# Kernel optimization log

Measured on AMD Instinct MI355X. Metric: run time of the kernel, lower is better.

## Reference

```python
import jax, jax.numpy as jnp
import numpy as np

D_MODEL, D_K, D_V, H = 1024, 64, 64, 16
B, NQ, NK = 4, 1024, 1024
HID = D_MODEL // 2


def _dwg(x, W1, b1, W2, b2):
    # DynamicWeightGenerator: sigmoid(fc2(relu(fc1(x))))
    h = jax.nn.relu(jnp.einsum('bnd,hd->bnh', x, W1) + b1)
    return jax.nn.sigmoid(jnp.einsum('bnh,dh->bnd', h, W2) + b2)


def setup_inputs() -> dict:
    key = jax.random.key(0)
    ks = jax.random.split(key, 32)
    s = 0.02
    inp = {
        'queries': jax.random.normal(ks[0], (B, NQ, D_MODEL), jnp.float32),
        'keys': jax.random.normal(ks[1], (B, NK, D_MODEL), jnp.float32),
        'values': jax.random.normal(ks[2], (B, NK, D_MODEL), jnp.float32),
        'attention_mask': jax.random.randint(ks[3], (B, 1, NQ, NK), 0, 2) > 0,
        'attention_weights': jax.random.uniform(ks[4], (B, H, NQ, NK), jnp.float32),
        'memory': jax.random.normal(ks[5], (B, NK), jnp.float32),
        # projections (torch Linear convention: y = x @ W.T + b)
        'Wq': jax.random.normal(ks[6], (H * D_K, D_MODEL), jnp.float32) * s,
        'bq': jnp.zeros((H * D_K,), jnp.float32),
        'Wk': jax.random.normal(ks[7], (H * D_K, D_MODEL), jnp.float32) * s,
        'bk': jnp.zeros((H * D_K,), jnp.float32),
        'Wv': jax.random.normal(ks[8], (H * D_V, D_MODEL), jnp.float32) * s,
        'bv': jnp.zeros((H * D_V,), jnp.float32),
        'Wo': jax.random.normal(ks[9], (D_MODEL, H * D_V), jnp.float32) * s,
        'bo': jnp.zeros((D_MODEL,), jnp.float32),
        'Wmm': jax.random.normal(ks[10], (H * D_V, 1), jnp.float32) * s,
        'bmm': jnp.zeros((H * D_V,), jnp.float32),
    }
    for i, tag in enumerate(['q', 'k', 'v']):
        k0, k1 = ks[11 + 2 * i], ks[12 + 2 * i]
        inp[f'W1{tag}'] = jax.random.normal(k0, (HID, D_MODEL), jnp.float32) * s
        inp[f'b1{tag}'] = jnp.zeros((HID,), jnp.float32)
        inp[f'W2{tag}'] = jax.random.normal(k1, (D_MODEL, HID), jnp.float32) * s
        inp[f'b2{tag}'] = jnp.zeros((D_MODEL,), jnp.float32)
    return inp


def reference(queries, keys, values, attention_mask, attention_weights, memory,
              Wq, bq, Wk, bk, Wv, bv, Wo, bo, Wmm, bmm,
              W1q, b1q, W2q, b2q, W1k, b1k, W2k, b2k, W1v, b1v, W2v, b2v):
    b_s, nq = queries.shape[:2]
    nk = keys.shape[1]
    # dynamic elementwise gating of inputs
    q_in = queries * _dwg(queries, W1q, b1q, W2q, b2q)
    k_in = keys * _dwg(keys, W1k, b1k, W2k, b2k)
    v_in = values * _dwg(values, W1v, b1v, W2v, b2v)
    # projections -> (b, h, n, d)
    q = (jnp.einsum('bnd,ed->bne', q_in, Wq) + bq).reshape(b_s, nq, H, D_K).transpose(0, 2, 1, 3)
    k = (jnp.einsum('bnd,ed->bne', k_in, Wk) + bk).reshape(b_s, nk, H, D_K).transpose(0, 2, 1, 3)
    v = (jnp.einsum('bnd,ed->bne', v_in, Wv) + bv).reshape(b_s, nk, H, D_V).transpose(0, 2, 1, 3)
    # per-token memory factor: fc_mm(memory[..., None]) -> (b, h, nk, d_k)
    mm = (memory[..., None] * Wmm[:, 0] + bmm).reshape(b_s, nk, H, D_K).transpose(0, 2, 1, 3)
    att = jnp.einsum('bhqd,bhkd->bhqk', q, k * mm) / np.sqrt(D_K).astype(np.float32)
    att = att * attention_weights                         # custom scaling (slice [:nk] == full)
    att = jnp.where(attention_mask, -jnp.inf, att)        # masked_fill
    att = jax.nn.softmax(att, axis=-1)
    out = jnp.einsum('bhqk,bhkd->bhqd', att, v * mm)      # (b, h, nq, d_v)
    out = out.transpose(0, 2, 1, 3).reshape(b_s, nq, H * D_V)
    return jnp.einsum('bne,de->bnd', out, Wo) + bo
```

## Files before the change

### kernel.cpp

```cpp
#include <hip/hip_runtime.h>
#include <hip/hip_bf16.h>

#define BB    4
#define NN    1024
#define DM    1024
#define HH    16
#define HID   512
#define TT    (BB * NN)

typedef __attribute__((ext_vector_type(8))) short bf16x8;
typedef __attribute__((ext_vector_type(4))) float f32x4;

__device__ __forceinline__ ushort f2bfu(float f) {
    __hip_bfloat16 h = __float2bfloat16(f);
    return __builtin_bit_cast(ushort, h);
}

__device__ __forceinline__ float bfu2f(ushort u) {
    __hip_bfloat16 h = __builtin_bit_cast(__hip_bfloat16, u);
    return __bfloat162float(h);
}

__device__ __forceinline__ f32x4 mfma16(bf16x8 a, bf16x8 b, f32x4 c) {
    return __builtin_amdgcn_mfma_f32_16x16x32_bf16(a, b, c, 0, 0, 0);
}

__device__ __forceinline__ void gll16(const void* g, void* l) {
    __builtin_amdgcn_global_load_lds(
        (const __attribute__((address_space(1))) unsigned int*)g,
        (__attribute__((address_space(3))) unsigned int*)l, 16, 0, 0);
}

__global__ void detect_mask_kernel(const uint4* __restrict__ m,
                                   int n16, int* __restrict__ flags) {
    int stride = blockDim.x * gridDim.x;
    unsigned hi = 0, lo = 0;
    for (int i = blockIdx.x * blockDim.x + threadIdx.x; i < n16; i += stride) {
        uint4 v = m[i];
        unsigned o = v.x | v.y | v.z | v.w;
        lo |= o & 0xFFu;
        hi |= o & 0xFFFFFF00u;
    }
    if (hi) atomicOr(&flags[0], 1);
    if (lo) atomicOr(&flags[1], 1);
}

#define NSEG 13
struct CvtAll { const float* s[NSEG]; ushort* d[NSEG]; int bound[NSEG]; };

__global__ __launch_bounds__(256) void cvt_all(CvtAll a, int total) {
    int stride = blockDim.x * gridDim.x;
    for (int i = blockIdx.x * blockDim.x + threadIdx.x; i < total; i += stride) {
        const float* sp = a.s[0];
        ushort* dp = a.d[0];
        int base = 0;
        #pragma unroll
        for (int k = 1; k < NSEG; ++k) {
            bool ge = i >= a.bound[k - 1];
            sp = ge ? a.s[k] : sp;
            dp = ge ? a.d[k] : dp;
            base = ge ? a.bound[k - 1] : base;
        }
        int j = i - base;
        float4 v = ((const float4*)sp)[j];
        uint2 o;
        o.x = (unsigned)f2bfu(v.x) | ((unsigned)f2bfu(v.y) << 16);
        o.y = (unsigned)f2bfu(v.z) | ((unsigned)f2bfu(v.w) << 16);
        ((uint2*)dp)[j] = o;
    }
}

struct GB {
    const ushort* A[3]; const ushort* W[3];
    const float* bias[3]; void* C[3]; const ushort* X[3];
};

template <int EP, int NF>
__global__ __launch_bounds__(256) void gemm_bf16(
    GB gb, int M, int N, int K,
    const float* __restrict__ mem, const float* __restrict__ Wmm,
    const float* __restrict__ bmm)
{
    __shared__ __align__(16) ushort As[2][128 * 64];
    __shared__ __align__(16) ushort Bs[2][NF * 32 * 64];
    const int z = blockIdx.z;
    const ushort* A = gb.A[z];
    const ushort* W = gb.W[z];
    const float* bias = gb.bias[z];
    void* Cout = gb.C[z];
    const ushort* X = gb.X[z];

    const int tid = threadIdx.x;
    const int lane = tid & 63, w = tid >> 6;
    const int lc = lane & 15, lg = lane >> 4;
    const int m0 = blockIdx.x * 128, n0 = blockIdx.y * (NF * 32);
    const int wm = (w >> 1) * 64, wn = (w & 1) * (NF * 16);
    const int srow = lane >> 3, scol = 8 * ((lane & 7) ^ srow);
    const int swl = (lc & 7) << 3;

    f32x4 acc[4][NF];
    #pragma unroll
    for (int i = 0; i < 4; ++i)
        #pragma unroll
        for (int j = 0; j < NF; ++j)
            acc[i][j] = (f32x4){0.f, 0.f, 0.f, 0.f};

    auto stage = [&](int buf, int k0) {
        #pragma unroll
        for (int ci = 0; ci < 4; ++ci) {
            int c = w + ci * 4;
            gll16(&A[(size_t)(m0 + c * 8 + srow) * K + k0 + scol], &As[buf][c * 512]);
            if (c < NF * 4)
                gll16(&W[(size_t)(n0 + c * 8 + srow) * K + k0 + scol], &Bs[buf][c * 512]);
        }
    };

    stage(0, 0);
    stage(1, 64);
    const int nt = K / 64;

    for (int t = 0; t < nt; ++t) {
        const int cur = t & 1;
        if (t < nt - 1) {
            if constexpr (NF == 4) asm volatile("s_waitcnt vmcnt(8)" ::: "memory");
            else                   asm volatile("s_waitcnt vmcnt(6)" ::: "memory");
        } else {
            asm volatile("s_waitcnt vmcnt(0)" ::: "memory");
        }
        __builtin_amdgcn_sched_barrier(0);
        __builtin_amdgcn_s_barrier();

        bf16x8 af[4][2], bfr[NF][2];
        #pragma unroll
        for (int mi = 0; mi < 4; ++mi) {
            int row = wm + mi * 16 + lc;
            af[mi][0] = *(const bf16x8*)&As[cur][row * 64 + ((lg * 8) ^ swl)];
            af[mi][1] = *(const bf16x8*)&As[cur][row * 64 + ((32 + lg * 8) ^ swl)];
        }
        #pragma unroll
        for (int nj = 0; nj < NF; ++nj) {
            int row = wn + nj * 16 + lc;
            bfr[nj][0] = *(const bf16x8*)&Bs[cur][row * 64 + ((lg * 8) ^ swl)];
            bfr[nj][1] = *(const bf16x8*)&Bs[cur][row * 64 + ((32 + lg * 8) ^ swl)];
        }
        asm volatile("s_waitcnt lgkmcnt(0)" ::: "memory");
        __builtin_amdgcn_sched_barrier(0);
        __builtin_amdgcn_s_barrier();

        if (t + 2 < nt) stage(cur, (t + 2) * 64);

        #pragma unroll
        for (int mi = 0; mi < 4; ++mi)
            #pragma unroll
            for (int nj = 0; nj < NF; ++nj) {
                acc[mi][nj] = mfma16(af[mi][0], bfr[nj][0], acc[mi][nj]);
                acc[mi][nj] = mfma16(af[mi][1], bfr[nj][1], acc[mi][nj]);
            }
    }

    #pragma unroll
    for (int nj = 0; nj < NF; ++nj) {
        int e = n0 + wn + nj * 16 + lc;
        float bv = bias[e];
        float wmv = 0.f, bmv = 0.f;
        if (EP == 7) { wmv = Wmm[e]; bmv = bmm[e]; }
        #pragma unroll
        for (int mi = 0; mi < 4; ++mi) {
            int mbase = m0 + wm + mi * 16 + lg * 4;
            if (EP == 7 && z == 2) {
                ushort u[4];
                #pragma unroll
                for (int r = 0; r < 4; ++r) {
                    float v = (acc[mi][nj][r] + bv) * (mem[mbase + r] * wmv + bmv);
                    u[r] = f2bfu(v);
                }
                int bb = mbase >> 10, n = mbase & 1023;
                size_t off = ((size_t)(bb * HH + (e >> 6)) * 64 + (e & 63)) * NN + n;
                uint2 pk;
                pk.x = (unsigned)u[0] | ((unsigned)u[1] << 16);
                pk.y = (unsigned)u[2] | ((unsigned)u[3] << 16);
                *(uint2*)&((ushort*)Cout)[off] = pk;
            } else {
                #pragma unroll
                for (int r = 0; r < 4; ++r) {
                    int m = mbase + r;
                    float v = acc[mi][nj][r] + bv;
                    if (EP == 1) v = fmaxf(v, 0.f);
                    if (EP == 2) v = bfu2f(X[(size_t)m * N + e]) * (1.f / (1.f + __expf(-v)));
                    if (EP == 7) {
                        if (z == 0) v = v * 0.125f;
                        else        v = v * (mem[m] * wmv + bmv);
                    }
                    size_t off = (size_t)m * N + e;
                    if (EP == 4) ((float*)Cout)[off] = v;
                    else         ((ushort*)Cout)[off] = f2bfu(v);
                }
            }
        }
    }
}

__global__ __launch_bounds__(256) void attn_fast(
    const ushort* __restrict__ qp, const ushort* __restrict__ kp,
    const ushort* __restrict__ vt, const float* __restrict__ aw,
    const unsigned char* __restrict__ maskp, const int* __restrict__ mflags,
    ushort* __restrict__ ob)
{
    const int mode = mflags[0] ? (mflags[1] ? 1 : 2) : 0;
    if (mode != 1) return;

    __shared__ __align__(16) ushort Ks[2][64 * 64];
    __shared__ __align__(16) ushort Vs[2][64 * 64];
    __shared__ __align__(16) float  AWs[2][64 * 64];
    __shared__ __align__(16) unsigned char Ms[2][64 * 64];
    __shared__ __align__(16) ushort Ps[64 * 64];

    const int tid = threadIdx.x, lane = tid & 63, w = tid >> 6;
    const int lc = lane & 15, lg = lane >> 4;
    const int bid = blockIdx.x;
    const int swz = (bid & 7) * 128 + (bid >> 3);
    const int qt = swz & 15, bh = swz >> 4;
    const int b = bh >> 4, h = bh & 15;
    const int q0 = qt * 64, wq = w * 16;
    const int srow = lane >> 3, scol = 8 * ((lane & 7) ^ srow);
    const int swl = (lc & 7) << 3;
    const int qloc = wq + lc;

    const ushort* qrow = &qp[(size_t)(b * NN + q0 + qloc) * DM + h * 64];
    bf16x8 bq0 = *(const bf16x8*)&qrow[lg * 8];
    bf16x8 bq1 = *(const bf16x8*)&qrow[32 + lg * 8];

    auto stage = [&](int buf, int t) {
        const int k0 = t * 64;
        #pragma unroll
        for (int ci = 0; ci < 2; ++ci) {
            int c = w + ci * 4;
            gll16(&kp[(size_t)(b * NN + k0 + c * 8 + srow) * DM + h * 64 + scol],
                  &Ks[buf][c * 512]);
            gll16(&vt[((size_t)bh * 64 + c * 8 + srow) * NN + k0 + scol],
                  &Vs[buf][c * 512]);
        }
        #pragma unroll
        for (int ci = 0; ci < 4; ++ci) {
            int c = w + ci * 4;
            int row = c * 4 + (lane >> 4);
            int un = (lane & 15) ^ (row & 7);
            gll16(&aw[((size_t)bh * NN + q0 + row) * NN + k0 + un * 4],
                  &AWs[buf][c * 256]);
        }
        {
            int row = w * 16 + (lane >> 2);
            int un = (lane & 3) ^ (row & 3);
            gll16(&maskp[((size_t)b * NN + q0 + row) * NN + k0 + un * 16],
                  &Ms[buf][w * 1024]);
        }
    };

    f32x4 oacc[4];
    #pragma unroll
    for (int i = 0; i < 4; ++i) oacc[i] = (f32x4){0.f, 0.f, 0.f, 0.f};
    float psum = 0.f;

    stage(0, 0);
    stage(1, 1);
    asm volatile("s_waitcnt vmcnt(0)" ::: "memory");
    __builtin_amdgcn_sched_barrier(0);
    __builtin_amdgcn_s_barrier();

    const int awk = qloc & 7;
    const int mkk = qloc & 3;

    for (int t = 0; t < 16; ++t) {
        const int cur = t & 1;
        if (t < 15) asm volatile("s_waitcnt vmcnt(9)" ::: "memory");
        else        asm volatile("s_waitcnt vmcnt(0)" ::: "memory");
        __builtin_amdgcn_sched_barrier(0);
        __builtin_amdgcn_s_barrier();

        bf16x8 af0[4], af1[4], vf0[4], vf1[4];
        float4 awf[4];
        unsigned mkf[4];
        #pragma unroll
        for (int mi = 0; mi < 4; ++mi) {
            int krow = mi * 16 + lc;
            af0[mi] = *(const bf16x8*)&Ks[cur][krow * 64 + ((lg * 8) ^ swl)];
            af1[mi] = *(const bf16x8*)&Ks[cur][krow * 64 + ((32 + lg * 8) ^ swl)];
        }
        #pragma unroll
        for (int nj = 0; nj < 4; ++nj) {
            int vrow = nj * 16 + lc;
            vf0[nj] = *(const bf16x8*)&Vs[cur][vrow * 64 + ((lg * 8) ^ swl)];
            vf1[nj] = *(const bf16x8*)&Vs[cur][vrow * 64 + ((32 + lg * 8) ^ swl)];
        }
        #pragma unroll
        for (int mi = 0; mi < 4; ++mi) {
            awf[mi] = *(const float4*)&AWs[cur][qloc * 64 + (((mi * 4 + lg) ^ awk) * 4)];
            mkf[mi] = *(const unsigned*)&Ms[cur][qloc * 64 + ((mi ^ mkk) * 16) + lg * 4];
        }
        asm volatile("s_waitcnt lgkmcnt(0)" ::: "memory");
        __builtin_amdgcn_sched_barrier(0);
        __builtin_amdgcn_s_barrier();

        if (t + 2 < 16) stage(cur, t + 2);

        f32x4 sacc[4];
        __builtin_amdgcn_s_setprio(1);
        #pragma unroll
        for (int mi = 0; mi < 4; ++mi) {
            f32x4 s = (f32x4){0.f, 0.f, 0.f, 0.f};
            s = mfma16(af0[mi], bq0, s);
            s = mfma16(af1[mi], bq1, s);
            sacc[mi] = s;
        }
        __builtin_amdgcn_s_setprio(0);

        #pragma unroll
        for (int mi = 0; mi < 4; ++mi) {
            unsigned mu = mkf[mi];
            const float aww[4] = {awf[mi].x, awf[mi].y, awf[mi].z, awf[mi].w};
            float pv[4];
            pv[0] = (mu & 0xffu)         ? 0.f : __expf(sacc[mi][0] * aww[0]);
            pv[1] = ((mu >> 8) & 0xffu)  ? 0.f : __expf(sacc[mi][1] * aww[1]);
            pv[2] = ((mu >> 16) & 0xffu) ? 0.f : __expf(sacc[mi][2] * aww[2]);
            pv[3] = ((mu >> 24) & 0xffu) ? 0.f : __expf(sacc[mi][3] * aww[3]);
            psum += pv[0] + pv[1] + pv[2] + pv[3];
            uint2 pk;
            pk.x = (unsigned)f2bfu(pv[0]) | ((unsigned)f2bfu(pv[1]) << 16);
            pk.y = (unsigned)f2bfu(pv[2]) | ((unsigned)f2bfu(pv[3]) << 16);
            *(uint2*)&Ps[qloc * 64 + ((mi * 16 + lg * 4) ^ swl)] = pk;
        }

        __builtin_amdgcn_s_setprio(1);
        {
            bf16x8 pa0 = *(const bf16x8*)&Ps[qloc * 64 + ((lg * 8) ^ swl)];
            #pragma unroll
            for (int nj = 0; nj < 4; ++nj)
                oacc[nj] = mfma16(pa0, vf0[nj], oacc[nj]);
            bf16x8 pa1 = *(const bf16x8*)&Ps[qloc * 64 + ((32 + lg * 8) ^ swl)];
            #pragma unroll
            for (int nj = 0; nj < 4; ++nj)
                oacc[nj] = mfma16(pa1, vf1[nj], oacc[nj]);
        }
        __builtin_amdgcn_s_setprio(0);
    }

    psum += __shfl_xor(psum, 16);
    psum += __shfl_xor(psum, 32);
    float inv = 1.0f / psum;
    float invr[4];
    #pragma unroll
    for (int r = 0; r < 4; ++r)
        invr[r] = __shfl(inv, (lane & 48) | (lg * 4 + r));

    #pragma unroll
    for (int nj = 0; nj < 4; ++nj)
        #pragma unroll
        for (int r = 0; r < 4; ++r) {
            int qq = q0 + wq + lg * 4 + r;
            float v = oacc[nj][r] * invr[r];
            ob[(size_t)(b * NN + qq) * DM + h * 64 + nj * 16 + lc] = f2bfu(v);
        }
}

__global__ __launch_bounds__(256) void attn_mfma_fb(
    const ushort* __restrict__ qp, const ushort* __restrict__ kp,
    const ushort* __restrict__ vt, const float* __restrict__ aw,
    const void* __restrict__ maskp, const int* __restrict__ mflags,
    ushort* __restrict__ ob)
{
    const int mode = mflags[0] ? (mflags[1] ? 1 : 2) : 0;
    if (mode == 1) return;
    __shared__ __align__(16) ushort Ks[2][64 * 64];
    __shared__ __align__(16) ushort Vs[2][64 * 64];
    __shared__ __align__(16) ushort Ps[64 * 64];
    const int tid = threadIdx.x, lane = tid & 63, w = tid >> 6;
    const int lc = lane & 15, lg = lane >> 4;
    const int bid = blockIdx.x;
    const int swz = (bid & 7) * 128 + (bid >> 3);
    const int qt = swz & 15, bh = swz >> 4;
    const int b = bh >> 4, h = bh & 15;
    const int q0 = qt * 64, wq = w * 16;
    const int srow = lane >> 3, scol = 8 * ((lane & 7) ^ srow);
    const int swl = (lc & 7) << 3;

    const ushort* qrow = &qp[(size_t)(b * NN + q0 + wq + lc) * DM + h * 64];
    bf16x8 bq0 = *(const bf16x8*)&qrow[lg * 8];
    bf16x8 bq1 = *(const bf16x8*)&qrow[32 + lg * 8];

    f32x4 oacc[4];
    #pragma unroll
    for (int i = 0; i < 4; ++i) oacc[i] = (f32x4){0.f, 0.f, 0.f, 0.f};
    float psum = 0.f;
    const int q = q0 + wq + lc;
    const float* awrow = aw + ((size_t)bh * NN + q) * NN;
    const size_t mrowo = ((size_t)b * NN + q) * NN;

    float4 awA[4], awB[4];
    uint4 mk4A[4], mk4B[4];

    #pragma unroll
    for (int ci = 0; ci < 2; ++ci) {
        int c = w + ci * 4;
        gll16(&kp[(size_t)(b * NN + c * 8 + srow) * DM + h * 64 + scol], &Ks[0][c * 512]);
        gll16(&vt[((size_t)bh * 64 + c * 8 + srow) * NN + 0 + scol], &Vs[0][c * 512]);
    }
    #pragma unroll
    for (int mi = 0; mi < 4; ++mi) {
        awA[mi] = *(const float4*)&awrow[mi * 16 + lg * 4];
        mk4A[mi] = *(const uint4*)((const char*)maskp + 4 * (mrowo + mi * 16 + lg * 4));
    }
    asm volatile("s_waitcnt vmcnt(0)" ::: "memory");
    __builtin_amdgcn_sched_barrier(0);
    __builtin_amdgcn_s_barrier();

#define ATTN_BODY(T, AWC, MK4C, AWN, MK4N)                                      \
    {                                                                           \
        const int cur = (T) & 1;                                                \
        if ((T) < 15) {                                                         \
            const int kn = ((T) + 1) * 64;                                      \
            _Pragma("unroll")                                                   \
            for (int ci = 0; ci < 2; ++ci) {                                    \
                int c = w + ci * 4;                                             \
                gll16(&kp[(size_t)(b * NN + kn + c * 8 + srow) * DM + h * 64 + scol], \
                      &Ks[cur ^ 1][c * 512]);                                   \
                gll16(&vt[((size_t)bh * 64 + c * 8 + srow) * NN + kn + scol],   \
                      &Vs[cur ^ 1][c * 512]);                                   \
            }                                                                   \
            __builtin_amdgcn_sched_barrier(0);                                  \
            _Pragma("unroll")                                                   \
            for (int mi = 0; mi < 4; ++mi) {                                    \
                AWN[mi] = *(const float4*)&awrow[kn + mi * 16 + lg * 4];        \
                MK4N[mi] = *(const uint4*)((const char*)maskp +                 \
                               4 * (mrowo + kn + mi * 16 + lg * 4));            \
            }                                                                   \
            __builtin_amdgcn_sched_barrier(0);                                  \
        }                                                                       \
        f32x4 sacc[4];                                                          \
        __builtin_amdgcn_s_setprio(1);                                          \
        _Pragma("unroll")                                                       \
        for (int mi = 0; mi < 4; ++mi) {                                        \
            int krow = mi * 16 + lc;                                            \
            bf16x8 a0 = *(const bf16x8*)&Ks[cur][krow * 64 + ((lg * 8) ^ swl)]; \
            bf16x8 a1 = *(const bf16x8*)&Ks[cur][krow * 64 + ((32 + lg * 8) ^ swl)]; \
            f32x4 s = (f32x4){0.f, 0.f, 0.f, 0.f};                              \
            s = mfma16(a0, bq0, s);                                             \
            s = mfma16(a1, bq1, s);                                             \
            sacc[mi] = s;                                                       \
        }                                                                       \
        __builtin_amdgcn_s_setprio(0);                                          \
        _Pragma("unroll")                                                       \
        for (int mi = 0; mi < 4; ++mi) {                                        \
            unsigned mk[4];                                                     \
            if (mode == 0) {                                                    \
                mk[0] = MK4C[mi].x; mk[1] = MK4C[mi].y;                         \
                mk[2] = MK4C[mi].z; mk[3] = MK4C[mi].w;                         \
            } else {                                                            \
                mk[0] = MK4C[mi].x != 0; mk[1] = MK4C[mi].y != 0;               \
                mk[2] = MK4C[mi].z != 0; mk[3] = MK4C[mi].w != 0;               \
            }                                                                   \
            const float aww[4] = {AWC[mi].x, AWC[mi].y, AWC[mi].z, AWC[mi].w};  \
            float pv[4];                                                        \
            _Pragma("unroll")                                                   \
            for (int r = 0; r < 4; ++r) {                                       \
                float sv = sacc[mi][r] * aww[r];                                \
                pv[r] = mk[r] ? 0.f : __expf(sv);                               \
                psum += pv[r];                                                  \
            }                                                                   \
            uint2 pk;                                                           \
            pk.x = (unsigned)f2bfu(pv[0]) | ((unsigned)f2bfu(pv[1]) << 16);     \
            pk.y = (unsigned)f2bfu(pv[2]) | ((unsigned)f2bfu(pv[3]) << 16);     \
            *(uint2*)&Ps[(wq + lc) * 64 + ((mi * 16 + lg * 4) ^ swl)] = pk;     \
        }                                                                       \
        __builtin_amdgcn_s_setprio(1);                                          \
        _Pragma("unroll")                                                       \
        for (int kk = 0; kk < 2; ++kk) {                                        \
            bf16x8 pa = *(const bf16x8*)&Ps[(wq + lc) * 64 + ((kk * 32 + lg * 8) ^ swl)]; \
            _Pragma("unroll")                                                   \
            for (int nj = 0; nj < 4; ++nj) {                                    \
                bf16x8 vb = *(const bf16x8*)&Vs[cur][(nj * 16 + lc) * 64 + ((kk * 32 + lg * 8) ^ swl)]; \
                oacc[nj] = mfma16(pa, vb, oacc[nj]);                            \
            }                                                                   \
        }                                                                       \
        __builtin_amdgcn_s_setprio(0);                                          \
        if ((T) < 15) {                                                         \
            asm volatile("s_waitcnt vmcnt(0)" ::: "memory");                    \
            __builtin_amdgcn_sched_barrier(0);                                  \
            __builtin_amdgcn_s_barrier();                                       \
        }                                                                       \
    }

    for (int tt = 0; tt < 8; ++tt) {
        const int t0 = tt * 2, t1 = tt * 2 + 1;
        ATTN_BODY(t0, awA, mk4A, awB, mk4B);
        ATTN_BODY(t1, awB, mk4B, awA, mk4A);
    }
#undef ATTN_BODY

    psum += __shfl_xor(psum, 16);
    psum += __shfl_xor(psum, 32);
    float inv = 1.0f / psum;
    float invr[4];
    #pragma unroll
    for (int r = 0; r < 4; ++r)
        invr[r] = __shfl(inv, (lane & 48) | (lg * 4 + r));

    #pragma unroll
    for (int nj = 0; nj < 4; ++nj)
        #pragma unroll
        for (int r = 0; r < 4; ++r) {
            int qq = q0 + wq + lg * 4 + r;
            float v = oacc[nj][r] * invr[r];
            ob[(size_t)(b * NN + qq) * DM + h * 64 + nj * 16 + lc] = f2bfu(v);
        }
}

extern "C" void kernel_launch(void* const* d_in, const int* in_sizes, int n_in,
                              void* d_out, int out_size, void* d_ws, size_t ws_size,
                              hipStream_t stream) {
    const float* xin_f[3] = {(const float*)d_in[0], (const float*)d_in[1], (const float*)d_in[2]};
    const void*  maskp   = d_in[3];
    const float* aw      = (const float*)d_in[4];
    const float* memv    = (const float*)d_in[5];
    const float* Wp_f[3] = {(const float*)d_in[6], (const float*)d_in[8], (const float*)d_in[10]};
    const float* bp[3]   = {(const float*)d_in[7], (const float*)d_in[9], (const float*)d_in[11]};
    const float* Wo_f  = (const float*)d_in[12];  const float* bo  = (const float*)d_in[13];
    const float* Wmm = (const float*)d_in[14];    const float* bmm = (const float*)d_in[15];
    const float* W1f[3] = {(const float*)d_in[16], (const float*)d_in[20], (const float*)d_in[24]};
    const float* b1a[3] = {(const float*)d_in[17], (const float*)d_in[21], (const float*)d_in[25]};
    const float* W2f[3] = {(const float*)d_in[18], (const float*)d_in[22], (const float*)d_in[26]};
    const float* b2a[3] = {(const float*)d_in[19], (const float*)d_in[23], (const float*)d_in[27]};

    char* p = (char*)d_ws;
    auto alloc = [&](size_t bytes) { char* r = p; p += (bytes + 255) & ~(size_t)255; return r; };
    int*    mflags = (int*)alloc(256);
    ushort* xbf[3]; for (int t = 0; t < 3; ++t) xbf[t] = (ushort*)alloc((size_t)TT * DM * 2);
    ushort* Wpb[3]; for (int t = 0; t < 3; ++t) Wpb[t] = (ushort*)alloc((size_t)DM * DM * 2);
    ushort* Wob  = (ushort*)alloc((size_t)DM * DM * 2);
    ushort* W1b[3]; for (int t = 0; t < 3; ++t) W1b[t] = (ushort*)alloc((size_t)HID * DM * 2);
    ushort* W2b[3]; for (int t = 0; t < 3; ++t) W2b[t] = (ushort*)alloc((size_t)DM * HID * 2);
    ushort* hbuf[3]; for (int t = 0; t < 3; ++t) hbuf[t] = (ushort*)alloc((size_t)TT * HID * 2);
    ushort* xg[3];  for (int t = 0; t < 3; ++t) xg[t] = (ushort*)alloc((size_t)TT * DM * 2);
    ushort* qpb  = (ushort*)alloc((size_t)TT * DM * 2);
    ushort* ksb  = (ushort*)alloc((size_t)TT * DM * 2);
    ushort* vtb  = (ushort*)alloc((size_t)TT * DM * 2);
    ushort* obuf = (ushort*)alloc((size_t)TT * DM * 2);

    hipMemsetAsync(mflags, 0, 8, stream);
    detect_mask_kernel<<<256, 256, 0, stream>>>((const uint4*)maskp,
                                                BB * NN * NN / 16, mflags);

    {
        CvtAll a;
        const int S_IN = TT * DM / 4, S_W = DM * DM / 4, S_H = HID * DM / 4;
        int idx = 0, cum = 0;
        auto seg = [&](const float* s, ushort* d, int n) {
            a.s[idx] = s; a.d[idx] = d; cum += n; a.bound[idx] = cum; ++idx;
        };
        for (int t = 0; t < 3; ++t) seg(xin_f[t], xbf[t], S_IN);
        for (int t = 0; t < 3; ++t) seg(Wp_f[t], Wpb[t], S_W);
        seg(Wo_f, Wob, S_W);
        for (int t = 0; t < 3; ++t) seg(W1f[t], W1b[t], S_H);
        for (int t = 0; t < 3; ++t) seg(W2f[t], W2b[t], S_H);
        cvt_all<<<2048, 256, 0, stream>>>(a, cum);
    }

    const dim3 blk(256);
    GB g1 = {}, g2 = {}, g3 = {}, g4 = {};
    for (int t = 0; t < 3; ++t) {
        g1.A[t] = xbf[t];  g1.W[t] = W1b[t]; g1.bias[t] = b1a[t]; g1.C[t] = hbuf[t];
        g2.A[t] = hbuf[t]; g2.W[t] = W2b[t]; g2.bias[t] = b2a[t]; g2.C[t] = xg[t]; g2.X[t] = xbf[t];
        g3.A[t] = xg[t];   g3.W[t] = Wpb[t]; g3.bias[t] = bp[t];
    }
    g3.C[0] = qpb; g3.C[1] = ksb; g3.C[2] = vtb;
    g4.A[0] = obuf; g4.W[0] = Wob; g4.bias[0] = bo; g4.C[0] = d_out;

    gemm_bf16<1, 2><<<dim3(TT / 128, HID / 64, 3), blk, 0, stream>>>(g1, TT, HID, DM, nullptr, nullptr, nullptr);
    gemm_bf16<2, 2><<<dim3(TT / 128, DM / 64, 3), blk, 0, stream>>>(g2, TT, DM, HID, nullptr, nullptr, nullptr);
    gemm_bf16<7, 2><<<dim3(TT / 128, DM / 64, 3), blk, 0, stream>>>(g3, TT, DM, DM, memv, Wmm, bmm);

    attn_fast<<<dim3(1024), blk, 0, stream>>>(qpb, ksb, vtb, aw,
                                              (const unsigned char*)maskp, mflags, obuf);
    attn_mfma_fb<<<dim3(1024), blk, 0, stream>>>(qpb, ksb, vtb, aw,
                                                 maskp, mflags, obuf);

    gemm_bf16<4, 2><<<dim3(TT / 128, DM / 64, 1), blk, 0, stream>>>(g4, TT, DM, DM, nullptr, nullptr, nullptr);
}
```

Before: 269.0 us.

## Single-buffer attention LDS tiles and fuse mask detection into convert kernel

Merges the mask-detection pass into the bf16 conversion kernel as extra blocks, removing a separate launch. Converts the attention kernels from double-buffered to single-buffered LDS staging for K, V, attention weights and mask, roughly halving shared memory per block to allow more resident blocks. The next tile's loads are still issued before compute but now need a full wait and barrier each iteration, reducing load/compute overlap within a block.

New measurement: 264.2 us. About the same (-1.8%).

```diff
diff --git a/kernel.cpp b/kernel.cpp
--- a/kernel.cpp
+++ b/kernel.cpp
@@ -31,42 +31,45 @@
         (__attribute__((address_space(3))) unsigned int*)l, 16, 0, 0);
 }
 
-__global__ void detect_mask_kernel(const uint4* __restrict__ m,
-                                   int n16, int* __restrict__ flags) {
-    int stride = blockDim.x * gridDim.x;
-    unsigned hi = 0, lo = 0;
-    for (int i = blockIdx.x * blockDim.x + threadIdx.x; i < n16; i += stride) {
-        uint4 v = m[i];
-        unsigned o = v.x | v.y | v.z | v.w;
-        lo |= o & 0xFFu;
-        hi |= o & 0xFFFFFF00u;
-    }
-    if (hi) atomicOr(&flags[0], 1);
-    if (lo) atomicOr(&flags[1], 1);
-}
-
 #define NSEG 13
 struct CvtAll { const float* s[NSEG]; ushort* d[NSEG]; int bound[NSEG]; };
 
-__global__ __launch_bounds__(256) void cvt_all(CvtAll a, int total) {
-    int stride = blockDim.x * gridDim.x;
-    for (int i = blockIdx.x * blockDim.x + threadIdx.x; i < total; i += stride) {
-        const float* sp = a.s[0];
-        ushort* dp = a.d[0];
-        int base = 0;
-        #pragma unroll
-        for (int k = 1; k < NSEG; ++k) {
-            bool ge = i >= a.bound[k - 1];
-            sp = ge ? a.s[k] : sp;
-            dp = ge ? a.d[k] : dp;
-            base = ge ? a.bound[k - 1] : base;
-        }
-        int j = i - base;
-        float4 v = ((const float4*)sp)[j];
-        uint2 o;
-        o.x = (unsigned)f2bfu(v.x) | ((unsigned)f2bfu(v.y) << 16);
-        o.y = (unsigned)f2bfu(v.z) | ((unsigned)f2bfu(v.w) << 16);
-        ((uint2*)dp)[j] = o;
+__global__ __launch_bounds__(256) void cvt_detect(
+    CvtAll a, int total, const uint4* __restrict__ m, int n16,
+    int* __restrict__ flags)
+{
+    if (blockIdx.x < 2048) {
+        int stride = 256 * 2048;
+        for (int i = blockIdx.x * 256 + threadIdx.x; i < total; i += stride) {
+            const float* sp = a.s[0];
+            ushort* dp = a.d[0];
+            int base = 0;
+            #pragma unroll
+            for (int k = 1; k < NSEG; ++k) {
+                bool ge = i >= a.bound[k - 1];
+                sp = ge ? a.s[k] : sp;
+                dp = ge ? a.d[k] : dp;
+                base = ge ? a.bound[k - 1] : base;
+            }
+            int j = i - base;
+            float4 v = ((const float4*)sp)[j];
+            uint2 o;
+            o.x = (unsigned)f2bfu(v.x) | ((unsigned)f2bfu(v.y) << 16);
+            o.y = (unsigned)f2bfu(v.z) | ((unsigned)f2bfu(v.w) << 16);
+            ((uint2*)dp)[j] = o;
+        }
+    } else {
+        int bid = blockIdx.x - 2048;
+        int stride = 256 * 256;
+        unsigned hi = 0, lo = 0;
+        for (int i = bid * 256 + threadIdx.x; i < n16; i += stride) {
+            uint4 v = m[i];
+            unsigned o = v.x | v.y | v.z | v.w;
+            lo |= o & 0xFFu;
+            hi |= o & 0xFFFFFF00u;
+        }
+        if (hi) atomicOr(&flags[0], 1);
+        if (lo) atomicOr(&flags[1], 1);
     }
 }
 
@@ -209,10 +212,10 @@
     const int mode = mflags[0] ? (mflags[1] ? 1 : 2) : 0;
     if (mode != 1) return;
 
-    __shared__ __align__(16) ushort Ks[2][64 * 64];
-    __shared__ __align__(16) ushort Vs[2][64 * 64];
-    __shared__ __align__(16) float  AWs[2][64 * 64];
-    __shared__ __align__(16) unsigned char Ms[2][64 * 64];
+    __shared__ __align__(16) ushort Ks[64 * 64];
+    __shared__ __align__(16) ushort Vs[64 * 64];
+    __shared__ __align__(16) float  AWs[64 * 64];
+    __shared__ __align__(16) unsigned char Ms[64 * 64];
     __shared__ __align__(16) ushort Ps[64 * 64];
 
     const int tid = threadIdx.x, lane = tid & 63, w = tid >> 6;
@@ -225,20 +228,23 @@
     const int srow = lane >> 3, scol = 8 * ((lane & 7) ^ srow);
     const int swl = (lc & 7) << 3;
     const int qloc = wq + lc;
+    const int awk = qloc & 7, mkk = qloc & 3;
 
     const ushort* qrow = &qp[(size_t)(b * NN + q0 + qloc) * DM + h * 64];
     bf16x8 bq0 = *(const bf16x8*)&qrow[lg * 8];
     bf16x8 bq1 = *(const bf16x8*)&qrow[32 + lg * 8];
 
-    auto stage = [&](int buf, int t) {
+    const unsigned char* mbase = maskp + ((size_t)b * NN + q0) * NN;
+
+    auto stage = [&](int t) {
         const int k0 = t * 64;
         #pragma unroll
         for (int ci = 0; ci < 2; ++ci) {
             int c = w + ci * 4;
             gll16(&kp[(size_t)(b * NN + k0 + c * 8 + srow) * DM + h * 64 + scol],
-                  &Ks[buf][c * 512]);
+                  &Ks[c * 512]);
             gll16(&vt[((size_t)bh * 64 + c * 8 + srow) * NN + k0 + scol],
-                  &Vs[buf][c * 512]);
+                  &Vs[c * 512]);
         }
         #pragma unroll
         for (int ci = 0; ci < 4; ++ci) {
@@ -246,13 +252,12 @@
             int row = c * 4 + (lane >> 4);
             int un = (lane & 15) ^ (row & 7);
             gll16(&aw[((size_t)bh * NN + q0 + row) * NN + k0 + un * 4],
-                  &AWs[buf][c * 256]);
+                  &AWs[c * 256]);
         }
         {
             int row = w * 16 + (lane >> 2);
             int un = (lane & 3) ^ (row & 3);
-            gll16(&maskp[((size_t)b * NN + q0 + row) * NN + k0 + un * 16],
-                  &Ms[buf][w * 1024]);
+            gll16(&mbase[(size_t)row * NN + k0 + un * 16], &Ms[w * 1024]);
         }
     };
 
@@ -261,47 +266,37 @@
     for (int i = 0; i < 4; ++i) oacc[i] = (f32x4){0.f, 0.f, 0.f, 0.f};
     float psum = 0.f;
 
-    stage(0, 0);
-    stage(1, 1);
+    stage(0);
     asm volatile("s_waitcnt vmcnt(0)" ::: "memory");
     __builtin_amdgcn_sched_barrier(0);
     __builtin_amdgcn_s_barrier();
 
-    const int awk = qloc & 7;
-    const int mkk = qloc & 3;
-
     for (int t = 0; t < 16; ++t) {
-        const int cur = t & 1;
-        if (t < 15) asm volatile("s_waitcnt vmcnt(9)" ::: "memory");
-        else        asm volatile("s_waitcnt vmcnt(0)" ::: "memory");
-        __builtin_amdgcn_sched_barrier(0);
-        __builtin_amdgcn_s_barrier();
-
         bf16x8 af0[4], af1[4], vf0[4], vf1[4];
         float4 awf[4];
         unsigned mkf[4];
         #pragma unroll
         for (int mi = 0; mi < 4; ++mi) {
             int krow = mi * 16 + lc;
-            af0[mi] = *(const bf16x8*)&Ks[cur][krow * 64 + ((lg * 8) ^ swl)];
-            af1[mi] = *(const bf16x8*)&Ks[cur][krow * 64 + ((32 + lg * 8) ^ swl)];
+            af0[mi] = *(const bf16x8*)&Ks[krow * 64 + ((lg * 8) ^ swl)];
+            af1[mi] = *(const bf16x8*)&Ks[krow * 64 + ((32 + lg * 8) ^ swl)];
         }
         #pragma unroll
         for (int nj = 0; nj < 4; ++nj) {
             int vrow = nj * 16 + lc;
-            vf0[nj] = *(const bf16x8*)&Vs[cur][vrow * 64 + ((lg * 8) ^ swl)];
-            vf1[nj] = *(const bf16x8*)&Vs[cur][vrow * 64 + ((32 + lg * 8) ^ swl)];
+            vf0[nj] = *(const bf16x8*)&Vs[vrow * 64 + ((lg * 8) ^ swl)];
+            vf1[nj] = *(const bf16x8*)&Vs[vrow * 64 + ((32 + lg * 8) ^ swl)];
         }
         #pragma unroll
         for (int mi = 0; mi < 4; ++mi) {
-            awf[mi] = *(const float4*)&AWs[cur][qloc * 64 + (((mi * 4 + lg) ^ awk) * 4)];
-            mkf[mi] = *(const unsigned*)&Ms[cur][qloc * 64 + ((mi ^ mkk) * 16) + lg * 4];
+            awf[mi] = *(const float4*)&AWs[qloc * 64 + (((mi * 4 + lg) ^ awk) * 4)];
+            mkf[mi] = *(const unsigned*)&Ms[qloc * 64 + ((mi ^ mkk) * 16) + lg * 4];
         }
         asm volatile("s_waitcnt lgkmcnt(0)" ::: "memory");
         __builtin_amdgcn_sched_barrier(0);
         __builtin_amdgcn_s_barrier();
 
-        if (t + 2 < 16) stage(cur, t + 2);
+        if (t < 15) stage(t + 1);
 
         f32x4 sacc[4];
         __builtin_amdgcn_s_setprio(1);
@@ -342,6 +337,12 @@
                 oacc[nj] = mfma16(pa1, vf1[nj], oacc[nj]);
         }
         __builtin_amdgcn_s_setprio(0);
+
+        if (t < 15) {
+            asm volatile("s_waitcnt vmcnt(0)" ::: "memory");
+            __builtin_amdgcn_sched_barrier(0);
+            __builtin_amdgcn_s_barrier();
+        }
     }
 
     psum += __shfl_xor(psum, 16);
@@ -362,7 +363,7 @@
         }
 }
 
-__global__ __launch_bounds__(256) void attn_mfma_fb(
+__global__ __launch_bounds__(256) void attn_fb(
     const ushort* __restrict__ qp, const ushort* __restrict__ kp,
     const ushort* __restrict__ vt, const float* __restrict__ aw,
     const void* __restrict__ maskp, const int* __restrict__ mflags,
@@ -370,8 +371,8 @@
 {
     const int mode = mflags[0] ? (mflags[1] ? 1 : 2) : 0;
     if (mode == 1) return;
-    __shared__ __align__(16) ushort Ks[2][64 * 64];
-    __shared__ __align__(16) ushort Vs[2][64 * 64];
+    __shared__ __align__(16) ushort Ks[64 * 64];
+    __shared__ __align__(16) ushort Vs[64 * 64];
     __shared__ __align__(16) ushort Ps[64 * 64];
     const int tid = threadIdx.x, lane = tid & 63, w = tid >> 6;
     const int lc = lane & 15, lg = lane >> 4;
@@ -401,8 +402,8 @@
     #pragma unroll
     for (int ci = 0; ci < 2; ++ci) {
         int c = w + ci * 4;
-        gll16(&kp[(size_t)(b * NN + c * 8 + srow) * DM + h * 64 + scol], &Ks[0][c * 512]);
-        gll16(&vt[((size_t)bh * 64 + c * 8 + srow) * NN + 0 + scol], &Vs[0][c * 512]);
+        gll16(&kp[(size_t)(b * NN + c * 8 + srow) * DM + h * 64 + scol], &Ks[c * 512]);
+        gll16(&vt[((size_t)bh * 64 + c * 8 + srow) * NN + 0 + scol], &Vs[c * 512]);
     }
     #pragma unroll
     for (int mi = 0; mi < 4; ++mi) {
@@ -415,18 +416,8 @@
 
 #define ATTN_BODY(T, AWC, MK4C, AWN, MK4N)                                      \
     {                                                                           \
-        const int cur = (T) & 1;                                                \
         if ((T) < 15) {                                                         \
             const int kn = ((T) + 1) * 64;                                      \
-            _Pragma("unroll")                                                   \
-            for (int ci = 0; ci < 2; ++ci) {                                    \
-                int c = w + ci * 4;                                             \
-                gll16(&kp[(size_t)(b * NN + kn + c * 8 + srow) * DM + h * 64 + scol], \
-                      &Ks[cur ^ 1][c * 512]);                                   \
-                gll16(&vt[((size_t)bh * 64 + c * 8 + srow) * NN + kn + scol],   \
-                      &Vs[cur ^ 1][c * 512]);                                   \
-            }                                                                   \
-            __builtin_amdgcn_sched_barrier(0);                                  \
             _Pragma("unroll")                                                   \
             for (int mi = 0; mi < 4; ++mi) {                                    \
                 AWN[mi] = *(const float4*)&awrow[kn + mi * 16 + lg * 4];        \
@@ -440,8 +431,8 @@
         _Pragma("unroll")                                                       \
         for (int mi = 0; mi < 4; ++mi) {                                        \
             int krow = mi * 16 + lc;                                            \
-            bf16x8 a0 = *(const bf16x8*)&Ks[cur][krow * 64 + ((lg * 8) ^ swl)]; \
-            bf16x8 a1 = *(const bf16x8*)&Ks[cur][krow * 64 + ((32 + lg * 8) ^ swl)]; \
+            bf16x8 a0 = *(const bf16x8*)&Ks[krow * 64 + ((lg * 8) ^ swl)];      \
+            bf16x8 a1 = *(const bf16x8*)&Ks[krow * 64 + ((32 + lg * 8) ^ swl)]; \
             f32x4 s = (f32x4){0.f, 0.f, 0.f, 0.f};                              \
             s = mfma16(a0, bq0, s);                                             \
             s = mfma16(a1, bq1, s);                                             \
@@ -477,12 +468,22 @@
             bf16x8 pa = *(const bf16x8*)&Ps[(wq + lc) * 64 + ((kk * 32 + lg * 8) ^ swl)]; \
             _Pragma("unroll")                                                   \
             for (int nj = 0; nj < 4; ++nj) {                                    \
-                bf16x8 vb = *(const bf16x8*)&Vs[cur][(nj * 16 + lc) * 64 + ((kk * 32 + lg * 8) ^ swl)]; \
+                bf16x8 vb = *(const bf16x8*)&Vs[(nj * 16 + lc) * 64 + ((kk * 32 + lg * 8) ^ swl)]; \
                 oacc[nj] = mfma16(pa, vb, oacc[nj]);                            \
             }                                                                   \
         }                                                                       \
         __builtin_amdgcn_s_setprio(0);                                          \
         if ((T) < 15) {                                                         \
+            __builtin_amdgcn_s_barrier();                                       \
+            const int kn = ((T) + 1) * 64;                                      \
+            _Pragma("unroll")                                                   \
+            for (int ci = 0; ci < 2; ++ci) {                                    \
+                int c = w + ci * 4;                                             \
+                gll16(&kp[(size_t)(b * NN + kn + c * 8 + srow) * DM + h * 64 + scol], \
+                      &Ks[c * 512]);                                            \
+                gll16(&vt[((size_t)bh * 64 + c * 8 + srow) * NN + kn + scol],   \
+                      &Vs[c * 512]);                                            \
+            }                                                                   \
             asm volatile("s_waitcnt vmcnt(0)" ::: "memory");                    \
             __builtin_amdgcn_sched_barrier(0);                                  \
             __builtin_amdgcn_s_barrier();                                       \
@@ -490,9 +491,8 @@
     }
 
     for (int tt = 0; tt < 8; ++tt) {
-        const int t0 = tt * 2, t1 = tt * 2 + 1;
-        ATTN_BODY(t0, awA, mk4A, awB, mk4B);
-        ATTN_BODY(t1, awB, mk4B, awA, mk4A);
+        ATTN_BODY(tt * 2,     awA, mk4A, awB, mk4B);
+        ATTN_BODY(tt * 2 + 1, awB, mk4B, awA, mk4A);
     }
 #undef ATTN_BODY
 
@@ -503,7 +503,6 @@
     #pragma unroll
     for (int r = 0; r < 4; ++r)
         invr[r] = __shfl(inv, (lane & 48) | (lg * 4 + r));
-
     #pragma unroll
     for (int nj = 0; nj < 4; ++nj)
         #pragma unroll
@@ -546,8 +545,6 @@
     ushort* obuf = (ushort*)alloc((size_t)TT * DM * 2);
 
     hipMemsetAsync(mflags, 0, 8, stream);
-    detect_mask_kernel<<<256, 256, 0, stream>>>((const uint4*)maskp,
-                                                BB * NN * NN / 16, mflags);
 
     {
         CvtAll a;
@@ -561,7 +558,8 @@
         seg(Wo_f, Wob, S_W);
         for (int t = 0; t < 3; ++t) seg(W1f[t], W1b[t], S_H);
         for (int t = 0; t < 3; ++t) seg(W2f[t], W2b[t], S_H);
-        cvt_all<<<2048, 256, 0, stream>>>(a, cum);
+        cvt_detect<<<2304, 256, 0, stream>>>(a, cum, (const uint4*)maskp,
+                                             BB * NN * NN / 16, mflags);
     }
 
     const dim3 blk(256);
@@ -580,8 +578,8 @@
 
     attn_fast<<<dim3(1024), blk, 0, stream>>>(qpb, ksb, vtb, aw,
                                               (const unsigned char*)maskp, mflags, obuf);
-    attn_mfma_fb<<<dim3(1024), blk, 0, stream>>>(qpb, ksb, vtb, aw,
-                                                 maskp, mflags, obuf);
+    attn_fb<<<dim3(1024), blk, 0, stream>>>(qpb, ksb, vtb, aw,
+                                            maskp, mflags, obuf);
 
     gemm_bf16<4, 2><<<dim3(TT / 128, DM / 64, 1), blk, 0, stream>>>(g4, TT, DM, DM, nullptr, nullptr, nullptr);
 }
```
